# Kernel optimization log

Measured on AMD Instinct MI355X. Metric: run time of the kernel, lower is better.

The kernel has to match this reference:

```python
import jax, jax.numpy as jnp
import numpy as np

B_GRAPHS = 64
N_PER = 2048          # nodes per graph (uniform -> total = B*N)
D = 256               # hidden_dim
U = D // 2            # GRU units per direction
L_LAYERS = 2


def setup_inputs() -> dict:
    key = jax.random.key(0)
    ks = jax.random.split(key, 8)
    T = B_GRAPHS * N_PER
    states = jax.random.normal(ks[0], (T, D), dtype=jnp.float32)
    rng = np.random.default_rng(0)
    pos = np.zeros((B_GRAPHS, N_PER), dtype=np.int32)
    for g in range(B_GRAPHS):
        mask = rng.random(N_PER) < 0.5
        L = int(mask.sum())
        pos[g, mask] = rng.permutation(L).astype(np.int32) + 1
    node_positions = jnp.asarray(pos.reshape(-1))
    graph_sizes = jnp.full((B_GRAPHS,), N_PER, dtype=jnp.int32)
    # GRU params (Keras GRU reset_after=True): kernel [D,3u], recurrent [u,3u], bias [2,3u]
    def mk(k):
        k1, k2, k3 = jax.random.split(k, 3)
        K = jax.random.normal(k1, (L_LAYERS, D, 3 * U), dtype=jnp.float32) * 0.06
        R = jax.random.normal(k2, (L_LAYERS, U, 3 * U), dtype=jnp.float32) * 0.06
        b = jax.random.normal(k3, (L_LAYERS, 2, 3 * U), dtype=jnp.float32) * 0.02
        return K, R, b
    K_fwd, R_fwd, b_fwd = mk(ks[1])
    K_bwd, R_bwd, b_bwd = mk(ks[2])
    return {"states": states, "node_positions": node_positions,
            "graph_sizes": graph_sizes, "training": 0,
            "K_fwd": K_fwd, "R_fwd": R_fwd, "b_fwd": b_fwd,
            "K_bwd": K_bwd, "R_bwd": R_bwd, "b_bwd": b_bwd}


def _gru_dir(seq, mask, K, R, b, reverse):
    # seq [B,S,Din], mask [B,S] -> outputs [B,S,U] (Keras GRU, reset_after=True)
    xs = jnp.swapaxes(seq, 0, 1)                 # [S,B,Din]
    ms = jnp.swapaxes(mask, 0, 1)                # [S,B]
    x_proj = xs @ K + b[0]                       # [S,B,3U] input projections
    Bsz = seq.shape[0]
    h0 = jnp.zeros((Bsz, U), seq.dtype)
    def step(h, inp):
        xp, m = inp
        hp = h @ R + b[1]                        # [B,3U]
        xz, xr, xh = jnp.split(xp, 3, axis=-1)
        hz, hr, hh = jnp.split(hp, 3, axis=-1)
        z = jax.nn.sigmoid(xz + hz)
        r = jax.nn.sigmoid(xr + hr)
        cand = jnp.tanh(xh + r * hh)
        h_new = z * h + (1.0 - z) * cand
        h = jnp.where(m[:, None], h_new, h)      # padded steps carry state
        return h, h
    _, ys = jax.lax.scan(step, h0, (x_proj, ms), reverse=reverse)
    return jnp.swapaxes(ys, 0, 1)


def _forward(states, node_positions, graph_sizes, training,
             K_fwd, R_fwd, b_fwd, K_bwd, R_bwd, b_bwd):
    T = states.shape[0]
    B = graph_sizes.shape[0]
    S = T // B  # max leaf-seq length (uniform graph sizes; bounds leaf count)
    gid = jnp.repeat(jnp.arange(B, dtype=jnp.int32), graph_sizes,
                     total_repeat_length=T)                      # [T]
    leaf = node_positions != 0                                   # [T]
    pos0 = node_positions - 1                                    # valid where leaf
    slot = jnp.where(leaf, pos0, S)                              # dump non-leaves
    # Pack ragged leaf sequences into dense [B,S,D] (extra slot S = trash)
    seq = jnp.zeros((B, S + 1, D), states.dtype).at[gid, slot].set(states)[:, :S]
    smask = jnp.zeros((B, S + 1), bool).at[gid, slot].set(leaf)[:, :S]
    drop_rate = 0.1 * float(training)
    x = seq
    key = jax.random.key(42)
    for l in range(L_LAYERS):
        yf = _gru_dir(x, smask, K_fwd[l], R_fwd[l], b_fwd[l], reverse=False)
        yb = _gru_dir(x, smask, K_bwd[l], R_bwd[l], b_bwd[l], reverse=True)
        x = jnp.concatenate([yf, yb], axis=-1)                   # [B,S,D]
        if drop_rate > 0.0:
            key, sub = jax.random.split(key)
            keep = jax.random.bernoulli(sub, 1.0 - drop_rate, x.shape)
            x = jnp.where(keep, x / (1.0 - drop_rate), 0.0)
    # Unpack: leaf nodes get RNN output, non-leaves keep original state
    gathered = x[gid, jnp.clip(pos0, 0)]                         # [T,D]
    return jnp.where(leaf[:, None], gathered, states)


def reference(states, node_positions, graph_sizes, training,
              K_fwd, R_fwd, b_fwd, K_bwd, R_bwd, b_bwd):
    return _forward(states, node_positions, graph_sizes, training,
                    K_fwd, R_fwd, b_fwd, K_bwd, R_bwd, b_bwd)
```

## Files before the change

kernel.cpp:

```cpp
#include <hip/hip_runtime.h>
#include <hip/hip_bf16.h>

#define B_GRAPHS 64
#define NPER     2048
#define T_NODES  (B_GRAPHS*NPER)
#define D_DIM    256
#define U_DIM    128
#define TU       384
#define XPW      768

typedef unsigned short ushortT;
typedef unsigned int   uint32;

typedef __attribute__((ext_vector_type(4))) float  f32x4;
typedef __attribute__((ext_vector_type(8))) __bf16 bf16x8;
typedef _Float16 f16;
typedef __attribute__((ext_vector_type(2))) _Float16 f16x2;

#define GAS __attribute__((address_space(1)))

static __device__ __forceinline__ ushortT f2bf(float f) {
  union { float f; uint32 u; } a; a.f = f;
  uint32 u = a.u;
  return (ushortT)((u + 0x7fffu + ((u >> 16) & 1u)) >> 16);
}
static __device__ __forceinline__ float bf2f(ushortT h) {
  union { uint32 u; float f; } a; a.u = ((uint32)h) << 16; return a.f;
}
static __device__ __forceinline__ f16x2 u2h(uint32 u) {
  union { uint32 u; f16x2 h; } x; x.u = u; return x.h;
}
static __device__ __forceinline__ float dot2f(f16x2 a, f16x2 b, float c) {
#if __has_builtin(__builtin_amdgcn_fdot2)
  return __builtin_amdgcn_fdot2(a, b, c, false);
#else
  return c + (float)a.x * (float)b.x + (float)a.y * (float)b.y;
#endif
}
static __device__ __forceinline__ float rcpf(float x) {
#if __has_builtin(__builtin_amdgcn_rcpf)
  return __builtin_amdgcn_rcpf(x);
#else
  return 1.0f / x;
#endif
}

static __device__ __forceinline__ ushortT gload_u16(const ushortT* p) {
  return *(const GAS ushortT*)p;
}
static __device__ __forceinline__ void gstore_u16(ushortT* p, ushortT v) {
  *(GAS ushortT*)p = v;
}

static __device__ __forceinline__ float xor32_sum(float v) {
  return v + __shfl_xor(v, 32);
}

__global__ __launch_bounds__(256) void prep_kernel(
    const float* __restrict__ Kf, const float* __restrict__ Kb,
    const float* __restrict__ bfw, const float* __restrict__ bbw,
    ushortT* __restrict__ Wt, float* __restrict__ b0)
{
  int idx = blockIdx.x * 256 + threadIdx.x;
  if (idx < 2 * XPW * D_DIM) {
    int l = idx / (XPW * D_DIM);
    int rem = idx % (XPW * D_DIM);
    int c = rem / D_DIM, k = rem % D_DIM;
    float v = (c < TU) ? Kf[(size_t)l * D_DIM * TU + (size_t)k * TU + c]
                       : Kb[(size_t)l * D_DIM * TU + (size_t)k * TU + (c - TU)];
    Wt[idx] = f2bf(v);
  } else {
    int i2 = idx - 2 * XPW * D_DIM;
    if (i2 < 2 * XPW) {
      int l = i2 / XPW, c = i2 % XPW;
      b0[i2] = (c < TU) ? bfw[l * 2 * TU + c] : bbw[l * 2 * TU + (c - TU)];
    }
  }
}

__global__ __launch_bounds__(256) void nodeofL_kernel(
    const int* __restrict__ pos, int* __restrict__ nodeof, int* __restrict__ L)
{
  int g = blockIdx.x, tid = threadIdx.x;
  __shared__ int red[256];
  int cnt = 0;
  for (int i = 0; i < NPER / 256; ++i) {
    int t = g * NPER + i * 256 + tid;
    int p = pos[t];
    if (p) { nodeof[g * NPER + p - 1] = t; cnt++; }
  }
  red[tid] = cnt; __syncthreads();
  for (int s = 128; s > 0; s >>= 1) {
    if (tid < s) red[tid] += red[tid + s];
    __syncthreads();
  }
  if (tid == 0) L[g] = red[0];
}

#if __has_builtin(__builtin_amdgcn_global_load_lds)
#define GLD_LDS(gsrc, ldst) \
  __builtin_amdgcn_global_load_lds((const GAS void*)(gsrc), \
                                   (__attribute__((address_space(3))) void*)(ldst), 16, 0, 0)
#define HAVE_GLD_LDS 1
#else
#define HAVE_GLD_LDS 0
#endif

__global__ __launch_bounds__(256) void gemm_kernel(
    const float* __restrict__ statesA, const ushortT* __restrict__ Adense,
    const ushortT* __restrict__ Wt, const float* __restrict__ b0,
    const int* __restrict__ nodeof, const int* __restrict__ L,
    ushortT* __restrict__ xp, int layer, int mode)
{
  int mblk = blockIdx.x, nblk = blockIdx.y;
  int g = mblk >> 4;
  int sBase = (mblk & 15) << 7;
  int Lg = L[g];
  if (sBase >= Lg) return;

  __shared__ __align__(16) ushortT As[128 * 32];
  __shared__ __align__(16) ushortT Bs[128 * 32];

  int tid = threadIdx.x;
  int lane = tid & 63, wid = tid >> 6;
  int wr = wid >> 1, wc = wid & 1;
  f32x4 acc[4][4];
  for (int i = 0; i < 4; i++) for (int n = 0; n < 4; n++) acc[i][n] = (f32x4){0.f,0.f,0.f,0.f};

  for (int kb = 0; kb < 8; ++kb) {
    __syncthreads();
    for (int c = 0; c < 2; ++c) {
      int flat = c * 4096 + tid * 16;
      int col = flat >> 6;
      size_t srcB = ((size_t)(layer * XPW + nblk * 128 + col)) * 512 + kb * 64 + (flat & 63);
#if HAVE_GLD_LDS
      GLD_LDS((const char*)Wt + srcB, (char*)Bs + c * 4096 + wid * 1024);
#else
      *(uint4*)((char*)Bs + flat) = *(const uint4*)((const char*)Wt + srcB);
#endif
    }
    if (mode) {
      for (int c = 0; c < 2; ++c) {
        int flat = c * 4096 + tid * 16;
        int row = flat >> 6;
        size_t srcA = ((size_t)(mblk * 128 + row)) * 512 + kb * 64 + (flat & 63);
#if HAVE_GLD_LDS
        GLD_LDS((const char*)Adense + srcA, (char*)As + c * 4096 + wid * 1024);
#else
        *(uint4*)((char*)As + flat) = *(const uint4*)((const char*)Adense + srcA);
#endif
      }
    } else {
      for (int c = 0; c < 2; ++c) {
        int flat = c * 4096 + tid * 16;
        int row = flat >> 6;
        int s = sBase + row;
        if (s < Lg) {
          int nt = nodeof[g * NPER + s];
          const float* sp = statesA + (size_t)nt * D_DIM + kb * 32 + ((flat & 63) >> 1);
          float4 u0 = *(const float4*)sp;
          float4 u1 = *(const float4*)(sp + 4);
          union { ushortT us[8]; uint4 v; } pk;
          pk.us[0] = f2bf(u0.x); pk.us[1] = f2bf(u0.y); pk.us[2] = f2bf(u0.z); pk.us[3] = f2bf(u0.w);
          pk.us[4] = f2bf(u1.x); pk.us[5] = f2bf(u1.y); pk.us[6] = f2bf(u1.z); pk.us[7] = f2bf(u1.w);
          *(uint4*)((char*)As + flat) = pk.v;
        }
      }
    }
    __syncthreads();

    bf16x8 af[4], bfr[4];
    for (int i = 0; i < 4; i++) {
      int off = (wr * 64 + i * 16 + (lane & 15)) * 32 + (lane >> 4) * 8;
      af[i] = *(const bf16x8*)&As[off];
    }
    for (int n = 0; n < 4; n++) {
      int off = (wc * 64 + n * 16 + (lane & 15)) * 32 + (lane >> 4) * 8;
      bfr[n] = *(const bf16x8*)&Bs[off];
    }
    for (int i = 0; i < 4; i++)
      for (int n = 0; n < 4; n++)
        acc[i][n] = __builtin_amdgcn_mfma_f32_16x16x32_bf16(af[i], bfr[n], acc[i][n], 0, 0, 0);
  }

  for (int n = 0; n < 4; n++) {
    int gcol = nblk * 128 + wc * 64 + n * 16 + (lane & 15);
    float bb = b0[layer * XPW + gcol];
    for (int i = 0; i < 4; i++) {
      int rowBase = mblk * 128 + wr * 64 + i * 16 + (lane >> 4) * 4;
      for (int v = 0; v < 4; v++)
        xp[(size_t)(rowBase + v) * XPW + gcol] = f2bf(acc[i][n][v] + bb);
    }
  }
}

__global__ __launch_bounds__(256) void rec_kernel(
    const ushortT* __restrict__ xp,
    const float* __restrict__ Rf, const float* __restrict__ Rb,
    const float* __restrict__ bfw, const float* __restrict__ bbw,
    const int* __restrict__ L, ushortT* __restrict__ y, int layer)
{
  int g = blockIdx.x, dir = blockIdx.y;
  int Lg = L[g];
  if (Lg == 0) return;
  int tid = threadIdx.x;
  int wave = tid >> 6, lane = tid & 63;
  int jl = lane & 31, half = lane >> 5;
  int j = wave * 32 + jl;

  __shared__ __align__(16) f16 hpk[2][128];

  const float* R  = (dir ? Rb : Rf) + (size_t)layer * U_DIM * TU;
  const float* b1 = (dir ? bbw : bfw) + layer * 2 * TU + TU;

  f16x2 rz[32], rg[32], rh[32];
  #pragma unroll
  for (int m = 0; m < 32; ++m) {
    int k = half * 64 + 2 * m;
    const float* p0 = R + (size_t)k * TU;
    const float* p1 = p0 + TU;
    f16x2 a, b, c;
    a.x = (f16)p0[j];        a.y = (f16)p1[j];
    b.x = (f16)p0[128 + j];  b.y = (f16)p1[128 + j];
    c.x = (f16)p0[256 + j];  c.y = (f16)p1[256 + j];
    rz[m] = a; rg[m] = b; rh[m] = c;
  }
  float bz = half ? 0.0f : b1[j];
  float br = half ? 0.0f : b1[128 + j];
  float bh = half ? 0.0f : b1[256 + j];

  if (tid < 128) hpk[0][tid] = (f16)0.0f;
  float hreg = 0.0f;
  __syncthreads();

  size_t xbase = (size_t)g * NPER * XPW + (size_t)dir * TU;
  ushortT xz0=0,xr0=0,xh0=0, xz1=0,xr1=0,xh1=0, xz2=0,xr2=0,xh2=0, xz3=0,xr3=0,xh3=0;
  {
    const ushortT* p;
    if (0 < Lg) { p = xp + xbase + (size_t)(dir ? Lg-1 : 0) * XPW;
                  xz0 = gload_u16(p+j); xr0 = gload_u16(p+128+j); xh0 = gload_u16(p+256+j); }
    if (1 < Lg) { p = xp + xbase + (size_t)(dir ? Lg-2 : 1) * XPW;
                  xz1 = gload_u16(p+j); xr1 = gload_u16(p+128+j); xh1 = gload_u16(p+256+j); }
    if (2 < Lg) { p = xp + xbase + (size_t)(dir ? Lg-3 : 2) * XPW;
                  xz2 = gload_u16(p+j); xr2 = gload_u16(p+128+j); xh2 = gload_u16(p+256+j); }
    if (3 < Lg) { p = xp + xbase + (size_t)(dir ? Lg-4 : 3) * XPW;
                  xz3 = gload_u16(p+j); xr3 = gload_u16(p+128+j); xh3 = gload_u16(p+256+j); }
  }

#define GRU_STEP(P, XZ, XR, XH, SS)                                              \
  {                                                                              \
    const int s_ = (SS);                                                         \
    float xzf = bf2f(XZ), xrf = bf2f(XR), xhf = bf2f(XH);                        \
    const int sp_ = s_ + 4;                                                      \
    if (sp_ < Lg) {                                                              \
      int pos2 = dir ? (Lg - 1 - sp_) : sp_;                                     \
      const ushortT* p_ = xp + xbase + (size_t)pos2 * XPW;                       \
      XZ = gload_u16(p_ + j);                                                    \
      XR = gload_u16(p_ + 128 + j);                                              \
      XH = gload_u16(p_ + 256 + j);                                              \
    }                                                                            \
    const uint4* hv = (const uint4*)&hpk[P][half * 64];                          \
    uint32 hw[32];                                                               \
    _Pragma("unroll")                                                            \
    for (int q8 = 0; q8 < 8; ++q8) {                                             \
      uint4 v_ = hv[q8];                                                         \
      hw[4*q8] = v_.x; hw[4*q8+1] = v_.y; hw[4*q8+2] = v_.z; hw[4*q8+3] = v_.w;  \
    }                                                                            \
    float az0 = bz, ar0 = br, ah0 = bh, az1 = 0.f, ar1 = 0.f, ah1 = 0.f;         \
    _Pragma("unroll")                                                            \
    for (int m = 0; m < 32; m += 2) {                                            \
      az0 = dot2f(u2h(hw[m]),   rz[m],   az0);                                   \
      ar0 = dot2f(u2h(hw[m]),   rg[m],   ar0);                                   \
      ah0 = dot2f(u2h(hw[m]),   rh[m],   ah0);                                   \
      az1 = dot2f(u2h(hw[m+1]), rz[m+1], az1);                                   \
      ar1 = dot2f(u2h(hw[m+1]), rg[m+1], ar1);                                   \
      ah1 = dot2f(u2h(hw[m+1]), rh[m+1], ah1);                                   \
    }                                                                            \
    float hz = xor32_sum(az0 + az1);                                             \
    float hr = xor32_sum(ar0 + ar1);                                             \
    float hh = xor32_sum(ah0 + ah1);                                             \
    float z = rcpf(1.0f + __expf(-(xzf + hz)));                                  \
    float r = rcpf(1.0f + __expf(-(xrf + hr)));                                  \
    float ch = xhf + r * hh;                                                     \
    float e = __expf(2.0f * __builtin_fabsf(ch));                                \
    float th = 1.0f - 2.0f * rcpf(e + 1.0f);                                     \
    float cand = __builtin_copysignf(th, ch);                                    \
    float hnew = cand + z * (hreg - cand);                                       \
    hreg = hnew;                                                                 \
    if (half) {                                                                  \
      int pos_ = dir ? (Lg - 1 - s_) : s_;                                       \
      gstore_u16(y + (size_t)(g * NPER + pos_) * D_DIM + dir * U_DIM + j,        \
                 f2bf(hnew));                                                    \
    } else {                                                                     \
      hpk[(P) ^ 1][j] = (f16)hnew;                                               \
    }                                                                            \
    asm volatile("s_waitcnt lgkmcnt(0)" ::: "memory");                           \
    __builtin_amdgcn_sched_barrier(0);                                           \
    __builtin_amdgcn_s_barrier();                                                \
    __builtin_amdgcn_sched_barrier(0);                                           \
  }

  for (int s = 0; s < Lg; s += 4) {
    GRU_STEP(0, xz0, xr0, xh0, s);
    if (s + 1 < Lg) GRU_STEP(1, xz1, xr1, xh1, s + 1);
    if (s + 2 < Lg) GRU_STEP(0, xz2, xr2, xh2, s + 2);
    if (s + 3 < Lg) GRU_STEP(1, xz3, xr3, xh3, s + 3);
  }
#undef GRU_STEP
}

__global__ __launch_bounds__(256) void unpack_kernel(
    const float* __restrict__ states, const int* __restrict__ pos,
    const ushortT* __restrict__ y, float* __restrict__ out)
{
  int node = blockIdx.x * 4 + (threadIdx.x >> 6);
  int lane = threadIdx.x & 63;
  int p = pos[node];
  int g = node >> 11;
  float4 v;
  if (p) {
    const ushortT* yp = y + (size_t)(g * NPER + p - 1) * D_DIM + lane * 4;
    v = make_float4(bf2f(yp[0]), bf2f(yp[1]), bf2f(yp[2]), bf2f(yp[3]));
  } else {
    v = *(const float4*)(states + (size_t)node * D_DIM + lane * 4);
  }
  *(float4*)(out + (size_t)node * D_DIM + lane * 4) = v;
}

extern "C" void kernel_launch(void* const* d_in, const int* in_sizes, int n_in,
                              void* d_out, int out_size, void* d_ws, size_t ws_size,
                              hipStream_t stream) {
  const float* states = (const float*)d_in[0];
  const int*   pos    = (const int*)d_in[1];
  const float* Kf  = (const float*)d_in[4];
  const float* Rf  = (const float*)d_in[5];
  const float* bfw = (const float*)d_in[6];
  const float* Kb  = (const float*)d_in[7];
  const float* Rb  = (const float*)d_in[8];
  const float* bbw = (const float*)d_in[9];

  char* ws = (char*)d_ws;
  int*     L      = (int*)(ws + 0);
  int*     nodeof = (int*)(ws + 256);
  ushortT* Wt     = (ushortT*)(ws + 524544);
  float*   b0     = (float*)(ws + 1310976);
  ushortT* xp     = (ushortT*)(ws + 1317120);
  ushortT* y      = (ushortT*)(ws + 202643712);

  prep_kernel<<<1542, 256, 0, stream>>>(Kf, Kb, bfw, bbw, Wt, b0);
  nodeofL_kernel<<<64, 256, 0, stream>>>(pos, nodeof, L);

  dim3 ggrid(1024, 6);
  dim3 rgrid(64, 2);

  gemm_kernel<<<ggrid, 256, 0, stream>>>(states, (const ushortT*)nullptr, Wt, b0, nodeof, L, xp, 0, 0);
  rec_kernel<<<rgrid, 256, 0, stream>>>(xp, Rf, Rb, bfw, bbw, L, y, 0);
  gemm_kernel<<<ggrid, 256, 0, stream>>>(states, y, Wt, b0, nodeof, L, xp, 1, 1);
  rec_kernel<<<rgrid, 256, 0, stream>>>(xp, Rf, Rb, bfw, bbw, L, y, 1);

  unpack_kernel<<<32768, 256, 0, stream>>>(states, pos, y, (float*)d_out);
}
```

Measured before the change: 1.268 ms.

## Interleave two graph recurrences per block to hide serial step latency

The recurrent kernel now processes two graphs per workgroup, interleaving their independent GRU steps so that one chain's dot products and activations can overlap the other's latency before a shared barrier. The grid is halved from 64 to 32 blocks per direction, and the number of barriers per pair of steps drops from two to one. In exchange each step does twice the serial work per block, the block runs until the longer of the two sequences finishes, and fewer CUs are occupied.

Result: slower. 2.212 ms (+74.5%).

```diff
diff --git a/kernel.cpp b/kernel.cpp
--- a/kernel.cpp
+++ b/kernel.cpp
@@ -200,15 +200,17 @@
     const float* __restrict__ bfw, const float* __restrict__ bbw,
     const int* __restrict__ L, ushortT* __restrict__ y, int layer)
 {
-  int g = blockIdx.x, dir = blockIdx.y;
-  int Lg = L[g];
-  if (Lg == 0) return;
+  int gp = blockIdx.x, dir = blockIdx.y;
+  int g0 = gp * 2, g1 = gp * 2 + 1;
+  int Lg0 = L[g0], Lg1 = L[g1];
+  int Lmax = Lg0 > Lg1 ? Lg0 : Lg1;
+  if (Lmax == 0) return;
   int tid = threadIdx.x;
   int wave = tid >> 6, lane = tid & 63;
   int jl = lane & 31, half = lane >> 5;
   int j = wave * 32 + jl;
 
-  __shared__ __align__(16) f16 hpk[2][128];
+  __shared__ __align__(16) f16 hpk[2][2][128];
 
   const float* R  = (dir ? Rb : Rf) + (size_t)layer * U_DIM * TU;
   const float* b1 = (dir ? bbw : bfw) + layer * 2 * TU + TU;
@@ -229,37 +231,48 @@
   float br = half ? 0.0f : b1[128 + j];
   float bh = half ? 0.0f : b1[256 + j];
 
-  if (tid < 128) hpk[0][tid] = (f16)0.0f;
-  float hreg = 0.0f;
+  if (tid < 128) { hpk[0][0][tid] = (f16)0.0f; hpk[1][0][tid] = (f16)0.0f; }
+  float hrega = 0.0f, hregb = 0.0f;
   __syncthreads();
 
-  size_t xbase = (size_t)g * NPER * XPW + (size_t)dir * TU;
-  ushortT xz0=0,xr0=0,xh0=0, xz1=0,xr1=0,xh1=0, xz2=0,xr2=0,xh2=0, xz3=0,xr3=0,xh3=0;
+  size_t xba = (size_t)g0 * NPER * XPW + (size_t)dir * TU;
+  size_t xbb = (size_t)g1 * NPER * XPW + (size_t)dir * TU;
+
+  ushortT Xza0=0,Xra0=0,Xha0=0, Xza1=0,Xra1=0,Xha1=0, Xza2=0,Xra2=0,Xha2=0, Xza3=0,Xra3=0,Xha3=0;
+  ushortT Xzb0=0,Xrb0=0,Xhb0=0, Xzb1=0,Xrb1=0,Xhb1=0, Xzb2=0,Xrb2=0,Xhb2=0, Xzb3=0,Xrb3=0,Xhb3=0;
   {
     const ushortT* p;
-    if (0 < Lg) { p = xp + xbase + (size_t)(dir ? Lg-1 : 0) * XPW;
-                  xz0 = gload_u16(p+j); xr0 = gload_u16(p+128+j); xh0 = gload_u16(p+256+j); }
-    if (1 < Lg) { p = xp + xbase + (size_t)(dir ? Lg-2 : 1) * XPW;
-                  xz1 = gload_u16(p+j); xr1 = gload_u16(p+128+j); xh1 = gload_u16(p+256+j); }
-    if (2 < Lg) { p = xp + xbase + (size_t)(dir ? Lg-3 : 2) * XPW;
-                  xz2 = gload_u16(p+j); xr2 = gload_u16(p+128+j); xh2 = gload_u16(p+256+j); }
-    if (3 < Lg) { p = xp + xbase + (size_t)(dir ? Lg-4 : 3) * XPW;
-                  xz3 = gload_u16(p+j); xr3 = gload_u16(p+128+j); xh3 = gload_u16(p+256+j); }
-  }
-
-#define GRU_STEP(P, XZ, XR, XH, SS)                                              \
-  {                                                                              \
+    if (0 < Lg0) { p = xp + xba + (size_t)(dir ? Lg0-1 : 0) * XPW;
+                   Xza0 = gload_u16(p+j); Xra0 = gload_u16(p+128+j); Xha0 = gload_u16(p+256+j); }
+    if (1 < Lg0) { p = xp + xba + (size_t)(dir ? Lg0-2 : 1) * XPW;
+                   Xza1 = gload_u16(p+j); Xra1 = gload_u16(p+128+j); Xha1 = gload_u16(p+256+j); }
+    if (2 < Lg0) { p = xp + xba + (size_t)(dir ? Lg0-3 : 2) * XPW;
+                   Xza2 = gload_u16(p+j); Xra2 = gload_u16(p+128+j); Xha2 = gload_u16(p+256+j); }
+    if (3 < Lg0) { p = xp + xba + (size_t)(dir ? Lg0-4 : 3) * XPW;
+                   Xza3 = gload_u16(p+j); Xra3 = gload_u16(p+128+j); Xha3 = gload_u16(p+256+j); }
+    if (0 < Lg1) { p = xp + xbb + (size_t)(dir ? Lg1-1 : 0) * XPW;
+                   Xzb0 = gload_u16(p+j); Xrb0 = gload_u16(p+128+j); Xhb0 = gload_u16(p+256+j); }
+    if (1 < Lg1) { p = xp + xbb + (size_t)(dir ? Lg1-2 : 1) * XPW;
+                   Xzb1 = gload_u16(p+j); Xrb1 = gload_u16(p+128+j); Xhb1 = gload_u16(p+256+j); }
+    if (2 < Lg1) { p = xp + xbb + (size_t)(dir ? Lg1-3 : 2) * XPW;
+                   Xzb2 = gload_u16(p+j); Xrb2 = gload_u16(p+128+j); Xhb2 = gload_u16(p+256+j); }
+    if (3 < Lg1) { p = xp + xbb + (size_t)(dir ? Lg1-4 : 3) * XPW;
+                   Xzb3 = gload_u16(p+j); Xrb3 = gload_u16(p+128+j); Xhb3 = gload_u16(p+256+j); }
+  }
+
+#define CHAIN_STEP(CH, P, XZ, XR, XH, SS, LG, XB, HR, GG)                        \
+  if ((SS) < (LG)) {                                                             \
     const int s_ = (SS);                                                         \
     float xzf = bf2f(XZ), xrf = bf2f(XR), xhf = bf2f(XH);                        \
     const int sp_ = s_ + 4;                                                      \
-    if (sp_ < Lg) {                                                              \
-      int pos2 = dir ? (Lg - 1 - sp_) : sp_;                                     \
-      const ushortT* p_ = xp + xbase + (size_t)pos2 * XPW;                       \
+    if (sp_ < (LG)) {                                                            \
+      int pos2 = dir ? ((LG) - 1 - sp_) : sp_;                                   \
+      const ushortT* p_ = xp + (XB) + (size_t)pos2 * XPW;                        \
       XZ = gload_u16(p_ + j);                                                    \
       XR = gload_u16(p_ + 128 + j);                                              \
       XH = gload_u16(p_ + 256 + j);                                              \
     }                                                                            \
-    const uint4* hv = (const uint4*)&hpk[P][half * 64];                          \
+    const uint4* hv = (const uint4*)&hpk[CH][P][half * 64];                      \
     uint32 hw[32];                                                               \
     _Pragma("unroll")                                                            \
     for (int q8 = 0; q8 < 8; ++q8) {                                             \
@@ -285,28 +298,39 @@
     float e = __expf(2.0f * __builtin_fabsf(ch));                                \
     float th = 1.0f - 2.0f * rcpf(e + 1.0f);                                     \
     float cand = __builtin_copysignf(th, ch);                                    \
-    float hnew = cand + z * (hreg - cand);                                       \
-    hreg = hnew;                                                                 \
+    float hnew = cand + z * ((HR) - cand);                                       \
+    (HR) = hnew;                                                                 \
     if (half) {                                                                  \
-      int pos_ = dir ? (Lg - 1 - s_) : s_;                                       \
-      gstore_u16(y + (size_t)(g * NPER + pos_) * D_DIM + dir * U_DIM + j,        \
+      int pos_ = dir ? ((LG) - 1 - s_) : s_;                                     \
+      gstore_u16(y + (size_t)((GG) * NPER + pos_) * D_DIM + dir * U_DIM + j,     \
                  f2bf(hnew));                                                    \
     } else {                                                                     \
-      hpk[(P) ^ 1][j] = (f16)hnew;                                               \
+      hpk[CH][(P) ^ 1][j] = (f16)hnew;                                           \
     }                                                                            \
+  }
+
+#define SYNC_STEP                                                                \
     asm volatile("s_waitcnt lgkmcnt(0)" ::: "memory");                           \
     __builtin_amdgcn_sched_barrier(0);                                           \
     __builtin_amdgcn_s_barrier();                                                \
-    __builtin_amdgcn_sched_barrier(0);                                           \
-  }
-
-  for (int s = 0; s < Lg; s += 4) {
-    GRU_STEP(0, xz0, xr0, xh0, s);
-    if (s + 1 < Lg) GRU_STEP(1, xz1, xr1, xh1, s + 1);
-    if (s + 2 < Lg) GRU_STEP(0, xz2, xr2, xh2, s + 2);
-    if (s + 3 < Lg) GRU_STEP(1, xz3, xr3, xh3, s + 3);
-  }
-#undef GRU_STEP
+    __builtin_amdgcn_sched_barrier(0);
+
+  for (int s = 0; s < Lmax; s += 4) {
+    CHAIN_STEP(0, 0, Xza0, Xra0, Xha0, s,     Lg0, xba, hrega, g0)
+    CHAIN_STEP(1, 0, Xzb0, Xrb0, Xhb0, s,     Lg1, xbb, hregb, g1)
+    SYNC_STEP
+    CHAIN_STEP(0, 1, Xza1, Xra1, Xha1, s + 1, Lg0, xba, hrega, g0)
+    CHAIN_STEP(1, 1, Xzb1, Xrb1, Xhb1, s + 1, Lg1, xbb, hregb, g1)
+    SYNC_STEP
+    CHAIN_STEP(0, 0, Xza2, Xra2, Xha2, s + 2, Lg0, xba, hrega, g0)
+    CHAIN_STEP(1, 0, Xzb2, Xrb2, Xhb2, s + 2, Lg1, xbb, hregb, g1)
+    SYNC_STEP
+    CHAIN_STEP(0, 1, Xza3, Xra3, Xha3, s + 3, Lg0, xba, hrega, g0)
+    CHAIN_STEP(1, 1, Xzb3, Xrb3, Xhb3, s + 3, Lg1, xbb, hregb, g1)
+    SYNC_STEP
+  }
+#undef CHAIN_STEP
+#undef SYNC_STEP
 }
 
 __global__ __launch_bounds__(256) void unpack_kernel(
@@ -351,7 +375,7 @@
   nodeofL_kernel<<<64, 256, 0, stream>>>(pos, nodeof, L);
 
   dim3 ggrid(1024, 6);
-  dim3 rgrid(64, 2);
+  dim3 rgrid(32, 2);
 
   gemm_kernel<<<ggrid, 256, 0, stream>>>(states, (const ushortT*)nullptr, Wt, b0, nodeof, L, xp, 0, 0);
   rec_kernel<<<rgrid, 256, 0, stream>>>(xp, Rf, Rb, bfw, bbw, L, y, 0);
```

## Pack two graph recurrence chains per block in GRU recurrent kernel

Applied to the files above, without the earlier changes.

The recurrent kernel now runs two graphs' GRU chains in one 512-thread block, each with its own shared hidden-state buffer. The grid is halved to 32x2 blocks and both chains step in lockstep up to the longer sequence, sharing one barrier per step. The intent is to double the waves per CU and interleave two independent dependency chains to hide latency. The cost is that the shorter chain sits idle at barriers until the longer one finishes, and the block now needs twice the register-resident R weights.

After: 2.034 ms. 60.5% more time.

```diff
diff --git a/kernel.cpp b/kernel.cpp
--- a/kernel.cpp
+++ b/kernel.cpp
@@ -194,21 +194,27 @@
   }
 }
 
-__global__ __launch_bounds__(256) void rec_kernel(
+__global__ __launch_bounds__(512) void rec_kernel(
     const ushortT* __restrict__ xp,
     const float* __restrict__ Rf, const float* __restrict__ Rb,
     const float* __restrict__ bfw, const float* __restrict__ bbw,
     const int* __restrict__ L, ushortT* __restrict__ y, int layer)
 {
-  int g = blockIdx.x, dir = blockIdx.y;
-  int Lg = L[g];
-  if (Lg == 0) return;
+  int gp = blockIdx.x, dir = blockIdx.y;
   int tid = threadIdx.x;
-  int wave = tid >> 6, lane = tid & 63;
+  int chain = tid >> 8;
+  int ctid = tid & 255;
+  int wave = ctid >> 6, lane = tid & 63;
   int jl = lane & 31, half = lane >> 5;
   int j = wave * 32 + jl;
 
-  __shared__ __align__(16) f16 hpk[2][128];
+  int g = gp * 2 + chain;
+  int Lg = L[g];
+  int Lg0 = L[gp * 2], Lg1 = L[gp * 2 + 1];
+  int Lmax = Lg0 > Lg1 ? Lg0 : Lg1;
+  if (Lmax == 0) return;
+
+  __shared__ __align__(16) f16 hpk[2][2][128];
 
   const float* R  = (dir ? Rb : Rf) + (size_t)layer * U_DIM * TU;
   const float* b1 = (dir ? bbw : bfw) + layer * 2 * TU + TU;
@@ -229,7 +235,7 @@
   float br = half ? 0.0f : b1[128 + j];
   float bh = half ? 0.0f : b1[256 + j];
 
-  if (tid < 128) hpk[0][tid] = (f16)0.0f;
+  if (ctid < 128) hpk[chain][0][ctid] = (f16)0.0f;
   float hreg = 0.0f;
   __syncthreads();
 
@@ -248,7 +254,7 @@
   }
 
 #define GRU_STEP(P, XZ, XR, XH, SS)                                              \
-  {                                                                              \
+  if ((SS) < Lg) {                                                               \
     const int s_ = (SS);                                                         \
     float xzf = bf2f(XZ), xrf = bf2f(XR), xhf = bf2f(XH);                        \
     const int sp_ = s_ + 4;                                                      \
@@ -259,7 +265,7 @@
       XR = gload_u16(p_ + 128 + j);                                              \
       XH = gload_u16(p_ + 256 + j);                                              \
     }                                                                            \
-    const uint4* hv = (const uint4*)&hpk[P][half * 64];                          \
+    const uint4* hv = (const uint4*)&hpk[chain][P][half * 64];                   \
     uint32 hw[32];                                                               \
     _Pragma("unroll")                                                            \
     for (int q8 = 0; q8 < 8; ++q8) {                                             \
@@ -292,21 +298,28 @@
       gstore_u16(y + (size_t)(g * NPER + pos_) * D_DIM + dir * U_DIM + j,        \
                  f2bf(hnew));                                                    \
     } else {                                                                     \
-      hpk[(P) ^ 1][j] = (f16)hnew;                                               \
+      hpk[chain][(P) ^ 1][j] = (f16)hnew;                                       \
     }                                                                            \
+  }
+
+#define SYNC_STEP                                                                \
     asm volatile("s_waitcnt lgkmcnt(0)" ::: "memory");                           \
     __builtin_amdgcn_sched_barrier(0);                                           \
     __builtin_amdgcn_s_barrier();                                                \
-    __builtin_amdgcn_sched_barrier(0);                                           \
-  }
-
-  for (int s = 0; s < Lg; s += 4) {
-    GRU_STEP(0, xz0, xr0, xh0, s);
-    if (s + 1 < Lg) GRU_STEP(1, xz1, xr1, xh1, s + 1);
-    if (s + 2 < Lg) GRU_STEP(0, xz2, xr2, xh2, s + 2);
-    if (s + 3 < Lg) GRU_STEP(1, xz3, xr3, xh3, s + 3);
+    __builtin_amdgcn_sched_barrier(0);
+
+  for (int s = 0; s < Lmax; s += 4) {
+    GRU_STEP(0, xz0, xr0, xh0, s)
+    SYNC_STEP
+    GRU_STEP(1, xz1, xr1, xh1, s + 1)
+    SYNC_STEP
+    GRU_STEP(0, xz2, xr2, xh2, s + 2)
+    SYNC_STEP
+    GRU_STEP(1, xz3, xr3, xh3, s + 3)
+    SYNC_STEP
   }
 #undef GRU_STEP
+#undef SYNC_STEP
 }
 
 __global__ __launch_bounds__(256) void unpack_kernel(
@@ -351,12 +364,12 @@
   nodeofL_kernel<<<64, 256, 0, stream>>>(pos, nodeof, L);
 
   dim3 ggrid(1024, 6);
-  dim3 rgrid(64, 2);
+  dim3 rgrid(32, 2);
 
   gemm_kernel<<<ggrid, 256, 0, stream>>>(states, (const ushortT*)nullptr, Wt, b0, nodeof, L, xp, 0, 0);
-  rec_kernel<<<rgrid, 256, 0, stream>>>(xp, Rf, Rb, bfw, bbw, L, y, 0);
+  rec_kernel<<<rgrid, 512, 0, stream>>>(xp, Rf, Rb, bfw, bbw, L, y, 0);
   gemm_kernel<<<ggrid, 256, 0, stream>>>(states, y, Wt, b0, nodeof, L, xp, 1, 1);
-  rec_kernel<<<rgrid, 256, 0, stream>>>(xp, Rf, Rb, bfw, bbw, L, y, 1);
+  rec_kernel<<<rgrid, 512, 0, stream>>>(xp, Rf, Rb, bfw, bbw, L, y, 1);
 
   unpack_kernel<<<32768, 256, 0, stream>>>(states, pos, y, (float*)d_out);
 }
```

## Use one thread per hidden unit in GRU recurrence and fold log2e into weights

Applied to the files above, without the earlier changes.

The recurrent kernel moves from 256 threads (two lanes per unit, each covering half of K, combined with a cross-lane shuffle) to 128 threads where each thread computes the full 128-length dot products for its unit. This removes the shuffle reductions and the half-select branch on every step. The cost is that each thread now holds twice as many recurrent weights in registers and runs a serial chain twice as long. Separately, log2(e) and 2·log2(e) are pre-multiplied into the input weights, biases and recurrent weights, so the sigmoid and tanh can use the hardware exp2 directly and skip a multiply. This rescaling changes rounding slightly because the scaled values are stored as bf16/f16.

Result: slower. 1.588 ms (+25.3%).

```diff
diff --git a/kernel.cpp b/kernel.cpp
--- a/kernel.cpp
+++ b/kernel.cpp
@@ -18,6 +18,7 @@
 typedef __attribute__((ext_vector_type(2))) _Float16 f16x2;
 
 #define GAS __attribute__((address_space(1)))
+#define LOG2E_F 1.4426950408889634f
 
 static __device__ __forceinline__ ushortT f2bf(float f) {
   union { float f; uint32 u; } a; a.f = f;
@@ -44,16 +45,18 @@
   return 1.0f / x;
 #endif
 }
-
+static __device__ __forceinline__ float exp2f_hw(float x) {
+#if __has_builtin(__builtin_amdgcn_exp2f)
+  return __builtin_amdgcn_exp2f(x);
+#else
+  return __expf(0.69314718055994531f * x);
+#endif
+}
 static __device__ __forceinline__ ushortT gload_u16(const ushortT* p) {
   return *(const GAS ushortT*)p;
 }
 static __device__ __forceinline__ void gstore_u16(ushortT* p, ushortT v) {
   *(GAS ushortT*)p = v;
-}
-
-static __device__ __forceinline__ float xor32_sum(float v) {
-  return v + __shfl_xor(v, 32);
 }
 
 __global__ __launch_bounds__(256) void prep_kernel(
@@ -68,12 +71,15 @@
     int c = rem / D_DIM, k = rem % D_DIM;
     float v = (c < TU) ? Kf[(size_t)l * D_DIM * TU + (size_t)k * TU + c]
                        : Kb[(size_t)l * D_DIM * TU + (size_t)k * TU + (c - TU)];
-    Wt[idx] = f2bf(v);
+    float sc = ((c % TU) < 256) ? LOG2E_F : 2.0f * LOG2E_F;
+    Wt[idx] = f2bf(v * sc);
   } else {
     int i2 = idx - 2 * XPW * D_DIM;
     if (i2 < 2 * XPW) {
       int l = i2 / XPW, c = i2 % XPW;
-      b0[i2] = (c < TU) ? bfw[l * 2 * TU + c] : bbw[l * 2 * TU + (c - TU)];
+      float v = (c < TU) ? bfw[l * 2 * TU + c] : bbw[l * 2 * TU + (c - TU)];
+      float sc = ((c % TU) < 256) ? LOG2E_F : 2.0f * LOG2E_F;
+      b0[i2] = v * sc;
     }
   }
 }
@@ -194,7 +200,7 @@
   }
 }
 
-__global__ __launch_bounds__(256) void rec_kernel(
+__global__ __launch_bounds__(128) void rec_kernel(
     const ushortT* __restrict__ xp,
     const float* __restrict__ Rf, const float* __restrict__ Rb,
     const float* __restrict__ bfw, const float* __restrict__ bbw,
@@ -203,33 +209,30 @@
   int g = blockIdx.x, dir = blockIdx.y;
   int Lg = L[g];
   if (Lg == 0) return;
-  int tid = threadIdx.x;
-  int wave = tid >> 6, lane = tid & 63;
-  int jl = lane & 31, half = lane >> 5;
-  int j = wave * 32 + jl;
+  int j = threadIdx.x;
 
   __shared__ __align__(16) f16 hpk[2][128];
 
-  const float* R  = (dir ? Rb : Rf) + (size_t)layer * U_DIM * TU;
-  const float* b1 = (dir ? bbw : bfw) + layer * 2 * TU + TU;
-
-  f16x2 rz[32], rg[32], rh[32];
+  const float* Rsrc = (dir ? Rb : Rf) + (size_t)layer * U_DIM * TU;
+  const float* b1p  = (dir ? bbw : bfw) + layer * 2 * TU + TU;
+
+  f16x2 rz[64], rg[64], rh[64];
   #pragma unroll
-  for (int m = 0; m < 32; ++m) {
-    int k = half * 64 + 2 * m;
-    const float* p0 = R + (size_t)k * TU;
+  for (int m = 0; m < 64; ++m) {
+    int k = 2 * m;
+    const float* p0 = Rsrc + (size_t)k * TU;
     const float* p1 = p0 + TU;
     f16x2 a, b, c;
-    a.x = (f16)p0[j];        a.y = (f16)p1[j];
-    b.x = (f16)p0[128 + j];  b.y = (f16)p1[128 + j];
-    c.x = (f16)p0[256 + j];  c.y = (f16)p1[256 + j];
+    a.x = (f16)(p0[j] * LOG2E_F);                a.y = (f16)(p1[j] * LOG2E_F);
+    b.x = (f16)(p0[128 + j] * LOG2E_F);          b.y = (f16)(p1[128 + j] * LOG2E_F);
+    c.x = (f16)(p0[256 + j] * (2.0f * LOG2E_F)); c.y = (f16)(p1[256 + j] * (2.0f * LOG2E_F));
     rz[m] = a; rg[m] = b; rh[m] = c;
   }
-  float bz = half ? 0.0f : b1[j];
-  float br = half ? 0.0f : b1[128 + j];
-  float bh = half ? 0.0f : b1[256 + j];
-
-  if (tid < 128) hpk[0][tid] = (f16)0.0f;
+  float bz = b1p[j] * LOG2E_F;
+  float br = b1p[128 + j] * LOG2E_F;
+  float bh = b1p[256 + j] * (2.0f * LOG2E_F);
+
+  hpk[0][j] = (f16)0.0f;
   float hreg = 0.0f;
   __syncthreads();
 
@@ -259,41 +262,40 @@
       XR = gload_u16(p_ + 128 + j);                                              \
       XH = gload_u16(p_ + 256 + j);                                              \
     }                                                                            \
-    const uint4* hv = (const uint4*)&hpk[P][half * 64];                          \
-    uint32 hw[32];                                                               \
-    _Pragma("unroll")                                                            \
-    for (int q8 = 0; q8 < 8; ++q8) {                                             \
-      uint4 v_ = hv[q8];                                                         \
-      hw[4*q8] = v_.x; hw[4*q8+1] = v_.y; hw[4*q8+2] = v_.z; hw[4*q8+3] = v_.w;  \
-    }                                                                            \
     float az0 = bz, ar0 = br, ah0 = bh, az1 = 0.f, ar1 = 0.f, ah1 = 0.f;         \
     _Pragma("unroll")                                                            \
-    for (int m = 0; m < 32; m += 2) {                                            \
-      az0 = dot2f(u2h(hw[m]),   rz[m],   az0);                                   \
-      ar0 = dot2f(u2h(hw[m]),   rg[m],   ar0);                                   \
-      ah0 = dot2f(u2h(hw[m]),   rh[m],   ah0);                                   \
-      az1 = dot2f(u2h(hw[m+1]), rz[m+1], az1);                                   \
-      ar1 = dot2f(u2h(hw[m+1]), rg[m+1], ar1);                                   \
-      ah1 = dot2f(u2h(hw[m+1]), rh[m+1], ah1);                                   \
+    for (int ho = 0; ho < 2; ++ho) {                                             \
+      const uint4* hv = (const uint4*)&hpk[P][ho * 64];                          \
+      uint32 hw[32];                                                             \
+      _Pragma("unroll")                                                          \
+      for (int q8 = 0; q8 < 8; ++q8) {                                           \
+        uint4 v_ = hv[q8];                                                       \
+        hw[4*q8] = v_.x; hw[4*q8+1] = v_.y; hw[4*q8+2] = v_.z; hw[4*q8+3] = v_.w;\
+      }                                                                          \
+      _Pragma("unroll")                                                          \
+      for (int m = 0; m < 32; m += 2) {                                          \
+        int mi = ho * 32 + m;                                                    \
+        az0 = dot2f(u2h(hw[m]),   rz[mi],   az0);                                \
+        ar0 = dot2f(u2h(hw[m]),   rg[mi],   ar0);                                \
+        ah0 = dot2f(u2h(hw[m]),   rh[mi],   ah0);                                \
+        az1 = dot2f(u2h(hw[m+1]), rz[mi+1], az1);                                \
+        ar1 = dot2f(u2h(hw[m+1]), rg[mi+1], ar1);                                \
+        ah1 = dot2f(u2h(hw[m+1]), rh[mi+1], ah1);                                \
+      }                                                                          \
     }                                                                            \
-    float hz = xor32_sum(az0 + az1);                                             \
-    float hr = xor32_sum(ar0 + ar1);                                             \
-    float hh = xor32_sum(ah0 + ah1);                                             \
-    float z = rcpf(1.0f + __expf(-(xzf + hz)));                                  \
-    float r = rcpf(1.0f + __expf(-(xrf + hr)));                                  \
-    float ch = xhf + r * hh;                                                     \
-    float e = __expf(2.0f * __builtin_fabsf(ch));                                \
+    float hz = az0 + az1, hr = ar0 + ar1, hh = ah0 + ah1;                        \
+    float z = rcpf(1.0f + exp2f_hw(-(xzf + hz)));                                \
+    float r = rcpf(1.0f + exp2f_hw(-(xrf + hr)));                                \
+    float a = xhf + r * hh;                                                      \
+    float e = exp2f_hw(__builtin_fabsf(a));                                      \
     float th = 1.0f - 2.0f * rcpf(e + 1.0f);                                     \
-    float cand = __builtin_copysignf(th, ch);                                    \
+    float cand = __builtin_copysignf(th, a);                                     \
     float hnew = cand + z * (hreg - cand);                                       \
     hreg = hnew;                                                                 \
-    if (half) {                                                                  \
-      int pos_ = dir ? (Lg - 1 - s_) : s_;                                       \
-      gstore_u16(y + (size_t)(g * NPER + pos_) * D_DIM + dir * U_DIM + j,        \
-                 f2bf(hnew));                                                    \
-    } else {                                                                     \
-      hpk[(P) ^ 1][j] = (f16)hnew;                                               \
-    }                                                                            \
+    int pos_ = dir ? (Lg - 1 - s_) : s_;                                         \
+    gstore_u16(y + (size_t)(g * NPER + pos_) * D_DIM + dir * U_DIM + j,          \
+               f2bf(hnew));                                                      \
+    hpk[(P) ^ 1][j] = (f16)hnew;                                                 \
     asm volatile("s_waitcnt lgkmcnt(0)" ::: "memory");                           \
     __builtin_amdgcn_sched_barrier(0);                                           \
     __builtin_amdgcn_s_barrier();                                                \
@@ -354,9 +356,9 @@
   dim3 rgrid(64, 2);
 
   gemm_kernel<<<ggrid, 256, 0, stream>>>(states, (const ushortT*)nullptr, Wt, b0, nodeof, L, xp, 0, 0);
-  rec_kernel<<<rgrid, 256, 0, stream>>>(xp, Rf, Rb, bfw, bbw, L, y, 0);
+  rec_kernel<<<rgrid, 128, 0, stream>>>(xp, Rf, Rb, bfw, bbw, L, y, 0);
   gemm_kernel<<<ggrid, 256, 0, stream>>>(states, y, Wt, b0, nodeof, L, xp, 1, 1);
-  rec_kernel<<<rgrid, 256, 0, stream>>>(xp, Rf, Rb, bfw, bbw, L, y, 1);
+  rec_kernel<<<rgrid, 128, 0, stream>>>(xp, Rf, Rb, bfw, bbw, L, y, 1);
 
   unpack_kernel<<<32768, 256, 0, stream>>>(states, pos, y, (float*)d_out);
 }
```
